# Optimization experiments

Measured on AMD Instinct MI355X. Metric: run time of the kernel, lower is better.

Reference implementation:

```python
import jax, jax.numpy as jnp
import numpy as np

H = 64  # hidden_size


def gru_layer(x, h0, W_ih, W_hh, b_ih, b_hh):
    """PyTorch-convention GRU layer. x: [B,T,D], h0: [B,H]. Returns ([B,T,H], [B,H])."""
    # Precompute input-side gate projections with one big GEMM: [B,T,3H]
    gx_all = jnp.einsum('btd,gd->btg', x, W_ih) + b_ih

    def step(h, gx):
        gh = h @ W_hh.T + b_hh                      # [B,3H]
        xr, xz, xn = jnp.split(gx, 3, axis=-1)
        hr, hz, hn = jnp.split(gh, 3, axis=-1)
        r = jax.nn.sigmoid(xr + hr)
        z = jax.nn.sigmoid(xz + hz)
        n = jnp.tanh(xn + r * hn)
        h_new = (1.0 - z) * n + z * h
        return h_new, h_new

    hT, hs = jax.lax.scan(step, h0, jnp.swapaxes(gx_all, 0, 1))  # hs: [T,B,H]
    return jnp.swapaxes(hs, 0, 1), hT


def setup_inputs() -> dict:
    key = jax.random.key(0)
    ks = jax.random.split(key, 16)
    B, T, D = 256, 2048, 1
    x = jax.random.normal(ks[0], (B, T, D), dtype=jnp.float32)
    h0 = jnp.zeros((2, B, H), dtype=jnp.float32)
    s = 1.0 / np.sqrt(H)
    # Layer 0: input_size=1
    W_ih0 = jax.random.normal(ks[1], (3 * H, D), dtype=jnp.float32) * s
    W_hh0 = jax.random.normal(ks[2], (3 * H, H), dtype=jnp.float32) * s
    b_ih0 = jnp.zeros((3 * H,), dtype=jnp.float32)
    b_hh0 = jnp.zeros((3 * H,), dtype=jnp.float32)
    # Layer 1: input_size=H
    W_ih1 = jax.random.normal(ks[3], (3 * H, H), dtype=jnp.float32) * s
    W_hh1 = jax.random.normal(ks[4], (3 * H, H), dtype=jnp.float32) * s
    b_ih1 = jnp.zeros((3 * H,), dtype=jnp.float32)
    b_hh1 = jnp.zeros((3 * H,), dtype=jnp.float32)
    # Head: Linear(H,H) -> ReLU -> Linear(H,1)
    Wh1 = jax.random.normal(ks[5], (H, H), dtype=jnp.float32) * s
    bh1 = jnp.zeros((H,), dtype=jnp.float32)
    Wh2 = jax.random.normal(ks[6], (1, H), dtype=jnp.float32) * s
    bh2 = jnp.zeros((1,), dtype=jnp.float32)
    return {"x": x, "h0": h0, "W_ih0": W_ih0, "W_hh0": W_hh0, "b_ih0": b_ih0,
            "b_hh0": b_hh0, "W_ih1": W_ih1, "W_hh1": W_hh1, "b_ih1": b_ih1,
            "b_hh1": b_hh1, "Wh1": Wh1, "bh1": bh1, "Wh2": Wh2, "bh2": bh2}


def reference(x, h0, W_ih0, W_hh0, b_ih0, b_hh0, W_ih1, W_hh1, b_ih1, b_hh1,
              Wh1, bh1, Wh2, bh2):
    z0, hT0 = gru_layer(x, h0[0], W_ih0, W_hh0, b_ih0, b_hh0)
    z1, hT1 = gru_layer(z0, h0[1], W_ih1, W_hh1, b_ih1, b_hh1)
    hT = jnp.stack([hT0, hT1], axis=0)           # [2,B,H]
    h = jax.nn.relu(jnp.einsum('bth,oh->bto', z1, Wh1) + bh1)
    y = jnp.einsum('bth,oh->bto', h, Wh2) + bh2  # [B,T,1]
    return (y, hT)
```

## Files before the change

### kernel.cpp

```cpp
#include <hip/hip_runtime.h>

#define HH 64
#define TT 2048
#define BB 256
#define YSZ (BB*TT)

__device__ __forceinline__ float sigmoid_f(float v) {
    return 1.0f / (1.0f + __expf(-v));
}
__device__ __forceinline__ float tanh_f(float v) {
    return 1.0f - 2.0f / (1.0f + __expf(2.0f * v));
}

#define AW(dst, val)  asm("v_accvgpr_write_b32 %0, %1" : "=a"(dst) : "v"(val))
#define AR(dst, src)  asm("v_accvgpr_read_b32 %0, %1"  : "=v"(dst) : "a"(src))
#define AMAC(acc, w, h) { float _t_; AR(_t_, w); acc = fmaf(_t_, (h), acc); }

__global__ __launch_bounds__(1024, 4)
void gru_fused(const float* __restrict__ x,
               const float* __restrict__ h0in,
               const float* __restrict__ W_ih0,
               const float* __restrict__ W_hh0,
               const float* __restrict__ b_ih0,
               const float* __restrict__ b_hh0,
               const float* __restrict__ W_ih1,
               const float* __restrict__ W_hh1,
               const float* __restrict__ b_ih1,
               const float* __restrict__ b_hh1,
               const float* __restrict__ Wh1,
               const float* __restrict__ bh1,
               const float* __restrict__ Wh2,
               const float* __restrict__ bh2,
               float* __restrict__ out)
{
    const int b   = blockIdx.x;
    const int tid = threadIdx.x;

    __shared__ __align__(16) float h0_lds[HH];
    __shared__ __align__(16) float h1_lds[HH];
    __shared__ __align__(16) float pg0[4 * 192];
    __shared__ __align__(16) float pg1[4 * 192];
    __shared__ __align__(16) float pg2[4 * 192];
    __shared__ __align__(16) float ph[4 * 64];
    __shared__ __align__(16) float x_lds[TT];

    {
        const float4* xs = reinterpret_cast<const float4*>(x + (size_t)b * TT);
        float4*       xd = reinterpret_cast<float4*>(x_lds);
        if (tid < TT / 4) xd[tid] = xs[tid];
    }
    if (tid < HH) {
        h0_lds[tid] = h0in[          b * HH + tid];
        h1_lds[tid] = h0in[BB * HH + b * HH + tid];
    }

    const bool is_gate = tid < 768;
    int q, t;
    if (is_gate) { q = tid / 192; t = tid - q * 192; }
    else         { q = (tid - 768) >> 6; t = (tid - 768) & 63; }

    float wA0x,wA0y,wA0z,wA0w, wA1x,wA1y,wA1z,wA1w,
          wA2x,wA2y,wA2z,wA2w, wA3x,wA3y,wA3z,wA3w;
    float wB0x,wB0y,wB0z,wB0w, wB1x,wB1y,wB1z,wB1w,
          wB2x,wB2y,wB2z,wB2w, wB3x,wB3y,wB3z,wB3w;
    float wC0x,wC0y,wC0z,wC0w, wC1x,wC1y,wC1z,wC1w,
          wC2x,wC2y,wC2z,wC2w, wC3x,wC3y,wC3z,wC3w;
    float bAa, bBa, bCa;

#define LOADM(P, ptr) { const float4* _p4 = reinterpret_cast<const float4*>(ptr); \
    float4 f4; \
    f4 = _p4[0]; AW(P##0x, f4.x); AW(P##0y, f4.y); AW(P##0z, f4.z); AW(P##0w, f4.w); \
    f4 = _p4[1]; AW(P##1x, f4.x); AW(P##1y, f4.y); AW(P##1z, f4.z); AW(P##1w, f4.w); \
    f4 = _p4[2]; AW(P##2x, f4.x); AW(P##2y, f4.y); AW(P##2z, f4.z); AW(P##2w, f4.w); \
    f4 = _p4[3]; AW(P##3x, f4.x); AW(P##3y, f4.y); AW(P##3z, f4.z); AW(P##3w, f4.w); }

    if (is_gate) {
        LOADM(wA, W_hh0 + t * HH + q * 16);
        LOADM(wB, W_ih1 + t * HH + q * 16);
        LOADM(wC, W_hh1 + t * HH + q * 16);
        float v0 = (q == 0) ? b_hh0[t] : 0.f;
        float v1 = (q == 0) ? b_ih1[t] : 0.f;
        float v2 = (q == 0) ? b_hh1[t] : 0.f;
        AW(bAa, v0); AW(bBa, v1); AW(bCa, v2);
    } else {
        LOADM(wA, Wh1 + t * HH + q * 16);
    }

    float wih0_r = 0.f, wih0_z = 0.f, wih0_n = 0.f;
    float bih0_r = 0.f, bih0_z = 0.f, bih0_n = 0.f;
    if (tid >= 64 && tid < 128) {
        const int j = tid - 64;
        wih0_r = W_ih0[j];       bih0_r = b_ih0[j];
        wih0_z = W_ih0[j + 64];  bih0_z = b_ih0[j + 64];
        wih0_n = W_ih0[j + 128]; bih0_n = b_ih0[j + 128];
    }
    float wh2r = 0.f, bh1r = 0.f, bh2s = 0.f;
    if (tid >= 128 && tid < 192) {
        const int j = tid - 128;
        wh2r = Wh2[j]; bh1r = bh1[j]; bh2s = bh2[0];
    }

    __syncthreads();

    const float4* h0q = reinterpret_cast<const float4*>(h0_lds) + (q << 2);
    const float4* h1q = reinterpret_cast<const float4*>(h1_lds) + (q << 2);

#define GQ(j) { float4 u = h0q[j]; float4 v = h1q[j]; \
    AMAC(a0, wA##j##x, u.x); AMAC(a1, wB##j##x, u.x); AMAC(a2, wC##j##x, v.x); \
    AMAC(a0, wA##j##y, u.y); AMAC(a1, wB##j##y, u.y); AMAC(a2, wC##j##y, v.y); \
    AMAC(a0, wA##j##z, u.z); AMAC(a1, wB##j##z, u.z); AMAC(a2, wC##j##z, v.z); \
    AMAC(a0, wA##j##w, u.w); AMAC(a1, wB##j##w, u.w); AMAC(a2, wC##j##w, v.w); }
#define HQ(j) { float4 v = h1q[j]; \
    AMAC(s, wA##j##x, v.x); AMAC(s, wA##j##y, v.y); \
    AMAC(s, wA##j##z, v.z); AMAC(s, wA##j##w, v.w); }

    for (int i = 0; i <= TT + 1; ++i) {
        if (is_gate) {
            float a0, a1, a2;
            AR(a0, bAa); AR(a1, bBa); AR(a2, bCa);
            GQ(0) GQ(1) GQ(2) GQ(3)
            pg0[q * 192 + t] = a0;
            pg1[q * 192 + t] = a1;
            pg2[q * 192 + t] = a2;
        } else {
            float s = 0.f;
            HQ(0) HQ(1) HQ(2) HQ(3)
            ph[q * 64 + t] = s;
        }
        __syncthreads();

        if (tid < 64) {
            const int j = tid;
            float sxr = 0.f, shr = 0.f, sxz = 0.f, shz = 0.f, sxn = 0.f, shn = 0.f;
            #pragma unroll
            for (int qq = 0; qq < 4; ++qq) {
                sxr += pg1[qq * 192 + j];       shr += pg2[qq * 192 + j];
                sxz += pg1[qq * 192 + j + 64];  shz += pg2[qq * 192 + j + 64];
                sxn += pg1[qq * 192 + j + 128]; shn += pg2[qq * 192 + j + 128];
            }
            float r = sigmoid_f(sxr + shr);
            float z = sigmoid_f(sxz + shz);
            float n = tanh_f(fmaf(r, shn, sxn));
            if (i >= 1 && i <= TT) {
                float hp = h1_lds[j];
                h1_lds[j] = fmaf(z, hp - n, n);
            }
        } else if (tid < 128) {
            const int j  = tid - 64;
            const int xi = (i < TT) ? i : (TT - 1);
            float g0 = 0.f, g1 = 0.f, g2 = 0.f;
            #pragma unroll
            for (int qq = 0; qq < 4; ++qq) {
                g0 += pg0[qq * 192 + j];
                g1 += pg0[qq * 192 + j + 64];
                g2 += pg0[qq * 192 + j + 128];
            }
            float xv = x_lds[xi];
            float r = sigmoid_f(fmaf(xv, wih0_r, bih0_r) + g0);
            float z = sigmoid_f(fmaf(xv, wih0_z, bih0_z) + g1);
            float n = tanh_f(fmaf(r, g2, fmaf(xv, wih0_n, bih0_n)));
            if (i < TT) {
                float hp = h0_lds[j];
                h0_lds[j] = fmaf(z, hp - n, n);
            }
        } else if (tid < 192) {
            const int j = tid - 128;
            float s = ph[j] + ph[64 + j] + ph[128 + j] + ph[192 + j] + bh1r;
            float p = fmaxf(s, 0.f) * wh2r;
            #pragma unroll
            for (int m = 1; m < 64; m <<= 1) p += __shfl_xor(p, m, 64);
            if (tid == 128 && i >= 2) out[(size_t)b * TT + (i - 2)] = p + bh2s;
        }
        __syncthreads();
    }

    if (tid < HH) {
        out[YSZ +           b * HH + tid] = h0_lds[tid];
        out[YSZ + BB * HH + b * HH + tid] = h1_lds[tid];
    }
}

extern "C" void kernel_launch(void* const* d_in, const int* in_sizes, int n_in,
                              void* d_out, int out_size, void* d_ws, size_t ws_size,
                              hipStream_t stream) {
    const float* x     = (const float*)d_in[0];
    const float* h0in  = (const float*)d_in[1];
    const float* W_ih0 = (const float*)d_in[2];
    const float* W_hh0 = (const float*)d_in[3];
    const float* b_ih0 = (const float*)d_in[4];
    const float* b_hh0 = (const float*)d_in[5];
    const float* W_ih1 = (const float*)d_in[6];
    const float* W_hh1 = (const float*)d_in[7];
    const float* b_ih1 = (const float*)d_in[8];
    const float* b_hh1 = (const float*)d_in[9];
    const float* Wh1   = (const float*)d_in[10];
    const float* bh1   = (const float*)d_in[11];
    const float* Wh2   = (const float*)d_in[12];
    const float* bh2   = (const float*)d_in[13];
    float* out = (float*)d_out;

    gru_fused<<<dim3(BB), dim3(1024), 0, stream>>>(
        x, h0in, W_ih0, W_hh0, b_ih0, b_hh0,
        W_ih1, W_hh1, b_ih1, b_hh1, Wh1, bh1, Wh2, bh2, out);
}
```

Measured before the change: 1.826 ms.

## Interleave K-split lanes and reduce partial gate sums with wave shuffles

Remaps threads so the four K-quarters of each gate row sit in adjacent lanes, then reduces the partial dot products with xor shuffles instead of writing four partial copies to LDS and summing them in the activation threads. Biases move out of the accumulator registers into the activation threads. This is meant to cut LDS traffic and the serial four-way sums on the critical path of each timestep. In exchange every gate thread runs extra shuffles and does a three-way select before storing, and weight loads are now strided across lanes.

```diff
diff --git a/kernel.cpp b/kernel.cpp
--- a/kernel.cpp
+++ b/kernel.cpp
@@ -38,10 +38,8 @@
 
     __shared__ __align__(16) float h0_lds[HH];
     __shared__ __align__(16) float h1_lds[HH];
-    __shared__ __align__(16) float pg0[4 * 192];
-    __shared__ __align__(16) float pg1[4 * 192];
-    __shared__ __align__(16) float pg2[4 * 192];
-    __shared__ __align__(16) float ph[4 * 64];
+    __shared__ __align__(16) float gbuf[3 * 200];
+    __shared__ __align__(16) float ph[HH];
     __shared__ __align__(16) float x_lds[TT];
 
     {
@@ -55,9 +53,8 @@
     }
 
     const bool is_gate = tid < 768;
-    int q, t;
-    if (is_gate) { q = tid / 192; t = tid - q * 192; }
-    else         { q = (tid - 768) >> 6; t = (tid - 768) & 63; }
+    const int  q = tid & 3;
+    const int  t = is_gate ? (tid >> 2) : ((tid - 768) >> 2);
 
     float wA0x,wA0y,wA0z,wA0w, wA1x,wA1y,wA1z,wA1w,
           wA2x,wA2y,wA2z,wA2w, wA3x,wA3y,wA3z,wA3w;
@@ -65,7 +62,6 @@
           wB2x,wB2y,wB2z,wB2w, wB3x,wB3y,wB3z,wB3w;
     float wC0x,wC0y,wC0z,wC0w, wC1x,wC1y,wC1z,wC1w,
           wC2x,wC2y,wC2z,wC2w, wC3x,wC3y,wC3z,wC3w;
-    float bAa, bBa, bCa;
 
 #define LOADM(P, ptr) { const float4* _p4 = reinterpret_cast<const float4*>(ptr); \
     float4 f4; \
@@ -78,21 +74,25 @@
         LOADM(wA, W_hh0 + t * HH + q * 16);
         LOADM(wB, W_ih1 + t * HH + q * 16);
         LOADM(wC, W_hh1 + t * HH + q * 16);
-        float v0 = (q == 0) ? b_hh0[t] : 0.f;
-        float v1 = (q == 0) ? b_ih1[t] : 0.f;
-        float v2 = (q == 0) ? b_hh1[t] : 0.f;
-        AW(bAa, v0); AW(bBa, v1); AW(bCa, v2);
     } else {
         LOADM(wA, Wh1 + t * HH + q * 16);
     }
 
+    float bxr = 0.f, bxz = 0.f, bxn = 0.f, bhr = 0.f, bhz = 0.f, bhn = 0.f;
+    if (tid < 64) {
+        const int j = tid;
+        bxr = b_ih1[j]; bxz = b_ih1[j + 64]; bxn = b_ih1[j + 128];
+        bhr = b_hh1[j]; bhz = b_hh1[j + 64]; bhn = b_hh1[j + 128];
+    }
     float wih0_r = 0.f, wih0_z = 0.f, wih0_n = 0.f;
     float bih0_r = 0.f, bih0_z = 0.f, bih0_n = 0.f;
+    float bh0r = 0.f, bh0z = 0.f, bh0n = 0.f;
     if (tid >= 64 && tid < 128) {
         const int j = tid - 64;
         wih0_r = W_ih0[j];       bih0_r = b_ih0[j];
         wih0_z = W_ih0[j + 64];  bih0_z = b_ih0[j + 64];
         wih0_n = W_ih0[j + 128]; bih0_n = b_ih0[j + 128];
+        bh0r = b_hh0[j]; bh0z = b_hh0[j + 64]; bh0n = b_hh0[j + 128];
     }
     float wh2r = 0.f, bh1r = 0.f, bh2s = 0.f;
     if (tid >= 128 && tid < 192) {
@@ -116,31 +116,34 @@
 
     for (int i = 0; i <= TT + 1; ++i) {
         if (is_gate) {
-            float a0, a1, a2;
-            AR(a0, bAa); AR(a1, bBa); AR(a2, bCa);
+            float a0 = 0.f, a1 = 0.f, a2 = 0.f;
             GQ(0) GQ(1) GQ(2) GQ(3)
-            pg0[q * 192 + t] = a0;
-            pg1[q * 192 + t] = a1;
-            pg2[q * 192 + t] = a2;
+            a0 += __shfl_xor(a0, 1, 64); a0 += __shfl_xor(a0, 2, 64);
+            a1 += __shfl_xor(a1, 1, 64); a1 += __shfl_xor(a1, 2, 64);
+            a2 += __shfl_xor(a2, 1, 64); a2 += __shfl_xor(a2, 2, 64);
+            if (q < 3) {
+                float v = (q == 0) ? a0 : (q == 1) ? a1 : a2;
+                gbuf[q * 200 + t] = v;
+            }
         } else {
             float s = 0.f;
             HQ(0) HQ(1) HQ(2) HQ(3)
-            ph[q * 64 + t] = s;
+            s += __shfl_xor(s, 1, 64); s += __shfl_xor(s, 2, 64);
+            if (q == 0) ph[t] = s;
         }
         __syncthreads();
 
         if (tid < 64) {
             const int j = tid;
-            float sxr = 0.f, shr = 0.f, sxz = 0.f, shz = 0.f, sxn = 0.f, shn = 0.f;
-            #pragma unroll
-            for (int qq = 0; qq < 4; ++qq) {
-                sxr += pg1[qq * 192 + j];       shr += pg2[qq * 192 + j];
-                sxz += pg1[qq * 192 + j + 64];  shz += pg2[qq * 192 + j + 64];
-                sxn += pg1[qq * 192 + j + 128]; shn += pg2[qq * 192 + j + 128];
-            }
-            float r = sigmoid_f(sxr + shr);
-            float z = sigmoid_f(sxz + shz);
-            float n = tanh_f(fmaf(r, shn, sxn));
+            float xr = gbuf[200 + j]       + bxr;
+            float xz = gbuf[200 + j + 64]  + bxz;
+            float xn = gbuf[200 + j + 128] + bxn;
+            float hr = gbuf[400 + j]       + bhr;
+            float hz = gbuf[400 + j + 64]  + bhz;
+            float hn = gbuf[400 + j + 128] + bhn;
+            float r = sigmoid_f(xr + hr);
+            float z = sigmoid_f(xz + hz);
+            float n = tanh_f(fmaf(r, hn, xn));
             if (i >= 1 && i <= TT) {
                 float hp = h1_lds[j];
                 h1_lds[j] = fmaf(z, hp - n, n);
@@ -148,13 +151,9 @@
         } else if (tid < 128) {
             const int j  = tid - 64;
             const int xi = (i < TT) ? i : (TT - 1);
-            float g0 = 0.f, g1 = 0.f, g2 = 0.f;
-            #pragma unroll
-            for (int qq = 0; qq < 4; ++qq) {
-                g0 += pg0[qq * 192 + j];
-                g1 += pg0[qq * 192 + j + 64];
-                g2 += pg0[qq * 192 + j + 128];
-            }
+            float g0 = gbuf[j]       + bh0r;
+            float g1 = gbuf[j + 64]  + bh0z;
+            float g2 = gbuf[j + 128] + bh0n;
             float xv = x_lds[xi];
             float r = sigmoid_f(fmaf(xv, wih0_r, bih0_r) + g0);
             float z = sigmoid_f(fmaf(xv, wih0_z, bih0_z) + g1);
@@ -165,7 +164,7 @@
             }
         } else if (tid < 192) {
             const int j = tid - 128;
-            float s = ph[j] + ph[64 + j] + ph[128 + j] + ph[192 + j] + bh1r;
+            float s = ph[j] + bh1r;
             float p = fmaxf(s, 0.f) * wh2r;
             #pragma unroll
             for (int m = 1; m < 64; m <<= 1) p += __shfl_xor(p, m, 64);
```

Result: slower. 2.070 ms (+13.3%).
